# Kernel tuning notes

Hardware: AMD Instinct MI355X
Metric: run time of the kernel (lower is better)

The kernel has to match this reference:

```python
import jax, jax.numpy as jnp
import numpy as np

N_NODES = 100000   # batch of target nodes
K = 10             # sampled neighbors per node (num_sample default)
VOCAB = 200000     # total graph nodes in embedding table
D = 128            # embed_dim


def setup_inputs() -> dict:
    key = jax.random.key(0)
    k1, k2, k3 = jax.random.split(key, 3)
    embed_table = jax.random.normal(k1, (VOCAB, D), dtype=jnp.float32)
    attn_w = jax.random.normal(k2, (D,), dtype=jnp.float32)
    neigh_idx = jax.random.randint(k3, (N_NODES, K), 0, VOCAB, dtype=jnp.int64)
    return {"embed_table": embed_table, "attn_w": attn_w, "neigh_idx": neigh_idx}


def reference(embed_table, attn_w, neigh_idx):
    # Gather neighbor embeddings: [N, K, D] (the irregular-access hot spot)
    feats = embed_table[neigh_idx]
    # attention_fc: Linear(D, 1, bias=False) -> scores [N, K]
    scores = jnp.einsum("nkd,d->nk", feats, attn_w)
    # softmax over the neighbor axis (dim=0 in the per-node torch loop == K here)
    weights = jax.nn.softmax(scores, axis=1)
    # attention-weighted sum of neighbor features -> [N, D]
    out = jnp.einsum("nk,nkd->nd", weights, feats)
    return out
```

## Files before the change

### kernel.cpp

```cpp
#include <hip/hip_runtime.h>
#include <math.h>


#define KNEIGH 10
#define DIM    128
#define QMAX   126.5f

__global__ __launch_bounds__(256) void convert_q8_kernel(
    const float*  __restrict__ table,
    const float*  __restrict__ attn_w,
    unsigned int* __restrict__ q8,
    float2*       __restrict__ aux,
    int vocab)
{
    const int gtid = blockIdx.x * blockDim.x + threadIdx.x;
    const int lane = threadIdx.x & 63;
    const int half = lane >> 5;
    const int sub  = lane & 31;
    const int row  = (gtid >> 6) * 2 + half;
    if (row >= vocab) return;

    const float4 f  = *(const float4*)(table + (size_t)row * DIM + sub * 4);
    const float4 w4 = *(const float4*)(attn_w + sub * 4);

    float p = f.x * w4.x + f.y * w4.y + f.z * w4.z + f.w * w4.w;
    float am = fmaxf(fmaxf(fabsf(f.x), fabsf(f.y)),
                     fmaxf(fabsf(f.z), fabsf(f.w)));
    #pragma unroll
    for (int off = 16; off >= 1; off >>= 1) {
        p  += __shfl_xor(p, off, 64);
        am  = fmaxf(am, __shfl_xor(am, off, 64));
    }

    const float scale = am * (1.0f / QMAX);
    const float inv   = (am > 0.f) ? (QMAX / am) : 0.f;

    const int q0 = (int)rintf(f.x * inv) + 128;
    const int q1 = (int)rintf(f.y * inv) + 128;
    const int q2 = (int)rintf(f.z * inv) + 128;
    const int q3 = (int)rintf(f.w * inv) + 128;
    q8[(size_t)row * 32 + sub] =
        (unsigned)q0 | ((unsigned)q1 << 8) | ((unsigned)q2 << 16) |
        ((unsigned)q3 << 24);

    if (sub == 0) aux[row] = make_float2(p, scale);
}

__global__ __launch_bounds__(256) void attn_gather_q8_kernel(
    const unsigned int* __restrict__ q8,
    const float2*       __restrict__ aux,
    const int*          __restrict__ idx,
    float*              __restrict__ out,
    int n_nodes)
{
    const int gtid = blockIdx.x * blockDim.x + threadIdx.x;
    const int wid  = gtid >> 6;
    const int n0   = wid * 2;
    if (n0 >= n_nodes) return;
    const int  n1   = n0 + 1;
    const bool has1 = (n1 < n_nodes);
    const int  lane = threadIdx.x & 63;
    const int  q    = lane >> 4;
    const int  sub  = lane & 15;

    const int b0 = __builtin_amdgcn_readfirstlane(n0) * KNEIGH;
    const int b1 = has1 ? b0 + KNEIGH : b0;

    const int ia0 = idx[b0+0], ia1 = idx[b0+1], ia2 = idx[b0+2], ia3 = idx[b0+3],
              ia4 = idx[b0+4], ia5 = idx[b0+5], ia6 = idx[b0+6], ia7 = idx[b0+7],
              ia8 = idx[b0+8], ia9 = idx[b0+9];
    const int ib0 = idx[b1+0], ib1 = idx[b1+1], ib2 = idx[b1+2], ib3 = idx[b1+3],
              ib4 = idx[b1+4], ib5 = idx[b1+5], ib6 = idx[b1+6], ib7 = idx[b1+7],
              ib8 = idx[b1+8], ib9 = idx[b1+9];

    const int r0 = (q == 0) ? ia0 : (q == 1) ? ia1 : (q == 2) ? ia2 : ia3;
    const int r1 = (q == 0) ? ia4 : (q == 1) ? ia5 : (q == 2) ? ia6 : ia7;
    const int r2 = (q == 0) ? ia8 : (q == 1) ? ia9 : (q == 2) ? ib0 : ib1;
    const int r3 = (q == 0) ? ib2 : (q == 1) ? ib3 : (q == 2) ? ib4 : ib5;
    const int r4 = (q == 0) ? ib6 : (q == 1) ? ib7 : (q == 2) ? ib8 : ib9;

    const uint2 g0 = *(const uint2*)(q8 + (size_t)r0 * 32 + sub * 2);
    const uint2 g1 = *(const uint2*)(q8 + (size_t)r1 * 32 + sub * 2);
    const uint2 g2 = *(const uint2*)(q8 + (size_t)r2 * 32 + sub * 2);
    const uint2 g3 = *(const uint2*)(q8 + (size_t)r3 * 32 + sub * 2);
    const uint2 g4 = *(const uint2*)(q8 + (size_t)r4 * 32 + sub * 2);

    const float2 aa0 = aux[ia0], aa1 = aux[ia1], aa2 = aux[ia2],
                 aa3 = aux[ia3], aa4 = aux[ia4], aa5 = aux[ia5],
                 aa6 = aux[ia6], aa7 = aux[ia7], aa8 = aux[ia8],
                 aa9 = aux[ia9];
    const float2 ab0 = aux[ib0], ab1 = aux[ib1], ab2 = aux[ib2],
                 ab3 = aux[ib3], ab4 = aux[ib4], ab5 = aux[ib5],
                 ab6 = aux[ib6], ab7 = aux[ib7], ab8 = aux[ib8],
                 ab9 = aux[ib9];

    float sa0 = aa0.x, sa1 = aa1.x, sa2 = aa2.x, sa3 = aa3.x, sa4 = aa4.x,
          sa5 = aa5.x, sa6 = aa6.x, sa7 = aa7.x, sa8 = aa8.x, sa9 = aa9.x;
    float ma = fmaxf(fmaxf(fmaxf(fmaxf(sa0, sa1), fmaxf(sa2, sa3)),
                           fmaxf(fmaxf(sa4, sa5), fmaxf(sa6, sa7))),
                     fmaxf(sa8, sa9));
    sa0 = __expf(sa0 - ma); sa1 = __expf(sa1 - ma); sa2 = __expf(sa2 - ma);
    sa3 = __expf(sa3 - ma); sa4 = __expf(sa4 - ma); sa5 = __expf(sa5 - ma);
    sa6 = __expf(sa6 - ma); sa7 = __expf(sa7 - ma); sa8 = __expf(sa8 - ma);
    sa9 = __expf(sa9 - ma);
    const float inva = 1.0f /
        (sa0 + sa1 + sa2 + sa3 + sa4 + sa5 + sa6 + sa7 + sa8 + sa9);

    float sb0 = ab0.x, sb1 = ab1.x, sb2 = ab2.x, sb3 = ab3.x, sb4 = ab4.x,
          sb5 = ab5.x, sb6 = ab6.x, sb7 = ab7.x, sb8 = ab8.x, sb9 = ab9.x;
    float mb = fmaxf(fmaxf(fmaxf(fmaxf(sb0, sb1), fmaxf(sb2, sb3)),
                           fmaxf(fmaxf(sb4, sb5), fmaxf(sb6, sb7))),
                     fmaxf(sb8, sb9));
    sb0 = __expf(sb0 - mb); sb1 = __expf(sb1 - mb); sb2 = __expf(sb2 - mb);
    sb3 = __expf(sb3 - mb); sb4 = __expf(sb4 - mb); sb5 = __expf(sb5 - mb);
    sb6 = __expf(sb6 - mb); sb7 = __expf(sb7 - mb); sb8 = __expf(sb8 - mb);
    sb9 = __expf(sb9 - mb);
    const float invb = 1.0f /
        (sb0 + sb1 + sb2 + sb3 + sb4 + sb5 + sb6 + sb7 + sb8 + sb9);

    const float ta0 = sa0 * inva * aa0.y, ta1 = sa1 * inva * aa1.y,
                ta2 = sa2 * inva * aa2.y, ta3 = sa3 * inva * aa3.y,
                ta4 = sa4 * inva * aa4.y, ta5 = sa5 * inva * aa5.y,
                ta6 = sa6 * inva * aa6.y, ta7 = sa7 * inva * aa7.y,
                ta8 = sa8 * inva * aa8.y, ta9 = sa9 * inva * aa9.y;
    const float tb0 = sb0 * invb * ab0.y, tb1 = sb1 * invb * ab1.y,
                tb2 = sb2 * invb * ab2.y, tb3 = sb3 * invb * ab3.y,
                tb4 = sb4 * invb * ab4.y, tb5 = sb5 * invb * ab5.y,
                tb6 = sb6 * invb * ab6.y, tb7 = sb7 * invb * ab7.y,
                tb8 = sb8 * invb * ab8.y, tb9 = sb9 * invb * ab9.y;

    const float Ca = -128.f * (ta0 + ta1 + ta2 + ta3 + ta4 +
                               ta5 + ta6 + ta7 + ta8 + ta9);
    const float Cb = -128.f * (tb0 + tb1 + tb2 + tb3 + tb4 +
                               tb5 + tb6 + tb7 + tb8 + tb9);

    const float w0 = (q == 0) ? ta0 : (q == 1) ? ta1 : (q == 2) ? ta2 : ta3;
    const float w1 = (q == 0) ? ta4 : (q == 1) ? ta5 : (q == 2) ? ta6 : ta7;
    const float w2 = (q == 0) ? ta8 : (q == 1) ? ta9 : (q == 2) ? tb0 : tb1;
    const float w3 = (q == 0) ? tb2 : (q == 1) ? tb3 : (q == 2) ? tb4 : tb5;
    const float w4 = (q == 0) ? tb6 : (q == 1) ? tb7 : (q == 2) ? tb8 : tb9;

    float a0=0.f,a1=0.f,a2=0.f,a3=0.f,a4=0.f,a5=0.f,a6=0.f,a7=0.f;
    float b0f=0.f,b1f=0.f,b2f=0.f,b3f=0.f,b4f=0.f,b5f=0.f,b6f=0.f,b7f=0.f;

    #define UNPK(G, W, A0,A1,A2,A3,A4,A5,A6,A7)                                \
        A0 = fmaf((W), (float)((G).x & 0xffu),         A0);                    \
        A1 = fmaf((W), (float)(((G).x >> 8) & 0xffu),  A1);                    \
        A2 = fmaf((W), (float)(((G).x >> 16) & 0xffu), A2);                    \
        A3 = fmaf((W), (float)((G).x >> 24),           A3);                    \
        A4 = fmaf((W), (float)((G).y & 0xffu),         A4);                    \
        A5 = fmaf((W), (float)(((G).y >> 8) & 0xffu),  A5);                    \
        A6 = fmaf((W), (float)(((G).y >> 16) & 0xffu), A6);                    \
        A7 = fmaf((W), (float)((G).y >> 24),           A7);

    UNPK(g0, w0, a0,a1,a2,a3,a4,a5,a6,a7)
    UNPK(g1, w1, a0,a1,a2,a3,a4,a5,a6,a7)
    {
        float c0=0.f,c1=0.f,c2=0.f,c3=0.f,c4=0.f,c5=0.f,c6=0.f,c7=0.f;
        UNPK(g2, w2, c0,c1,c2,c3,c4,c5,c6,c7)
        const bool lo = (q < 2);
        a0 += lo ? c0 : 0.f; a1 += lo ? c1 : 0.f; a2 += lo ? c2 : 0.f;
        a3 += lo ? c3 : 0.f; a4 += lo ? c4 : 0.f; a5 += lo ? c5 : 0.f;
        a6 += lo ? c6 : 0.f; a7 += lo ? c7 : 0.f;
        b0f += lo ? 0.f : c0; b1f += lo ? 0.f : c1; b2f += lo ? 0.f : c2;
        b3f += lo ? 0.f : c3; b4f += lo ? 0.f : c4; b5f += lo ? 0.f : c5;
        b6f += lo ? 0.f : c6; b7f += lo ? 0.f : c7;
    }
    UNPK(g3, w3, b0f,b1f,b2f,b3f,b4f,b5f,b6f,b7f)
    UNPK(g4, w4, b0f,b1f,b2f,b3f,b4f,b5f,b6f,b7f)
    #undef UNPK

    #define RED(X) X += __shfl_xor(X, 16, 64); X += __shfl_xor(X, 32, 64);
    RED(a0) RED(a1) RED(a2) RED(a3) RED(a4) RED(a5) RED(a6) RED(a7)
    RED(b0f) RED(b1f) RED(b2f) RED(b3f) RED(b4f) RED(b5f) RED(b6f) RED(b7f)
    #undef RED

    if (q == 0) {
        float* p = out + (size_t)n0 * DIM + sub * 8;
        *(float4*)(p)     = make_float4(a0 + Ca, a1 + Ca, a2 + Ca, a3 + Ca);
        *(float4*)(p + 4) = make_float4(a4 + Ca, a5 + Ca, a6 + Ca, a7 + Ca);
    } else if (q == 1 && has1) {
        float* p = out + (size_t)n1 * DIM + sub * 8;
        *(float4*)(p)     = make_float4(b0f + Cb, b1f + Cb, b2f + Cb, b3f + Cb);
        *(float4*)(p + 4) = make_float4(b4f + Cb, b5f + Cb, b6f + Cb, b7f + Cb);
    }
}

__global__ __launch_bounds__(256) void attn_agg_fp32_kernel(
    const float* __restrict__ table,
    const float* __restrict__ attn_w,
    const int*   __restrict__ idx,
    float*       __restrict__ out,
    int n_nodes)
{
    const int gtid = blockIdx.x * blockDim.x + threadIdx.x;
    const int node = gtid >> 6;
    const int lane = threadIdx.x & 63;
    if (node >= n_nodes) return;

    const float2 wv = *(const float2*)(attn_w + lane * 2);
    int my_idx = 0;
    if (lane < KNEIGH) my_idx = idx[node * KNEIGH + lane];

    float2 f[KNEIGH];
    float  s[KNEIGH];
    #pragma unroll
    for (int k = 0; k < KNEIGH; ++k) {
        const int id = __shfl(my_idx, k, 64);
        f[k] = *(const float2*)(table + (size_t)id * DIM + lane * 2);
        float p = f[k].x * wv.x + f[k].y * wv.y;
        #pragma unroll
        for (int off = 32; off >= 1; off >>= 1)
            p += __shfl_xor(p, off, 64);
        s[k] = p;
    }
    float m = s[0];
    #pragma unroll
    for (int k = 1; k < KNEIGH; ++k) m = fmaxf(m, s[k]);
    float denom = 0.f;
    #pragma unroll
    for (int k = 0; k < KNEIGH; ++k) { s[k] = __expf(s[k] - m); denom += s[k]; }
    const float inv = 1.0f / denom;
    float2 acc = make_float2(0.f, 0.f);
    #pragma unroll
    for (int k = 0; k < KNEIGH; ++k) {
        const float wk = s[k] * inv;
        acc.x = fmaf(wk, f[k].x, acc.x);
        acc.y = fmaf(wk, f[k].y, acc.y);
    }
    *(float2*)(out + (size_t)node * DIM + lane * 2) = acc;
}

extern "C" void kernel_launch(void* const* d_in, const int* in_sizes, int n_in,
                              void* d_out, int out_size, void* d_ws, size_t ws_size,
                              hipStream_t stream) {
    const float* table  = (const float*)d_in[0];
    const float* attn_w = (const float*)d_in[1];
    const int*   idx    = (const int*)d_in[2];
    float*       out    = (float*)d_out;

    const int vocab   = in_sizes[0] / DIM;
    const int n_nodes = in_sizes[2] / KNEIGH;

    const size_t q8_bytes = (size_t)vocab * DIM;
    const size_t need     = q8_bytes + (size_t)vocab * sizeof(float2);

    if (ws_size >= need) {
        unsigned int* q8  = (unsigned int*)d_ws;
        float2*       aux = (float2*)((char*)d_ws + q8_bytes);

        const int waves1  = (vocab + 1) / 2;
        const int blocks1 = (waves1 + 3) / 4;
        convert_q8_kernel<<<blocks1, 256, 0, stream>>>(
            table, attn_w, q8, aux, vocab);

        const int waves2  = (n_nodes + 1) / 2;
        const int blocks2 = (waves2 + 3) / 4;
        attn_gather_q8_kernel<<<blocks2, 256, 0, stream>>>(
            q8, aux, idx, out, n_nodes);
    } else {
        const int blocks = (n_nodes + 3) / 4;
        attn_agg_fp32_kernel<<<blocks, 256, 0, stream>>>(
            table, attn_w, idx, out, n_nodes);
    }
}
```

Before: 197.2 us.

## Split softmax weight computation into separate per-node kernel before gather

Moves the per-node softmax over the neighbor scores into a new kernel that runs one thread per node and writes normalized, scale-folded weights plus an offset constant to a workspace buffer. The gather kernel then reads 12 precomputed floats per node instead of redundantly computing 20 aux gathers, exps and reductions in every lane of the wave. The gather kernel also gets a launch-bounds occupancy hint. The cost is an extra kernel launch and an extra round trip through workspace memory for the weights.

Measured after the change: 194.7 us. No clear change (-1.3%).

```diff
diff --git a/kernel.cpp b/kernel.cpp
--- a/kernel.cpp
+++ b/kernel.cpp
@@ -2,9 +2,10 @@
 #include <math.h>
 
 
-#define KNEIGH 10
-#define DIM    128
-#define QMAX   126.5f
+#define KNEIGH  10
+#define DIM     128
+#define QMAX    126.5f
+#define WSTRIDE 12
 
 __global__ __launch_bounds__(256) void convert_q8_kernel(
     const float*  __restrict__ table,
@@ -46,16 +47,56 @@
     if (sub == 0) aux[row] = make_float2(p, scale);
 }
 
-__global__ __launch_bounds__(256) void attn_gather_q8_kernel(
+__global__ __launch_bounds__(256) void weights_kernel(
+    const float2* __restrict__ aux,
+    const int*    __restrict__ idx,
+    float*        __restrict__ wt,
+    int n_nodes)
+{
+    const int node = blockIdx.x * blockDim.x + threadIdx.x;
+    if (node >= n_nodes) return;
+
+    const int2* ip = (const int2*)(idx + (size_t)node * KNEIGH);
+    const int2 i01 = ip[0], i23 = ip[1], i45 = ip[2], i67 = ip[3], i89 = ip[4];
+
+    const float2 a0 = aux[i01.x], a1 = aux[i01.y], a2 = aux[i23.x],
+                 a3 = aux[i23.y], a4 = aux[i45.x], a5 = aux[i45.y],
+                 a6 = aux[i67.x], a7 = aux[i67.y], a8 = aux[i89.x],
+                 a9 = aux[i89.y];
+
+    const float m = fmaxf(fmaxf(fmaxf(fmaxf(a0.x, a1.x), fmaxf(a2.x, a3.x)),
+                                fmaxf(fmaxf(a4.x, a5.x), fmaxf(a6.x, a7.x))),
+                          fmaxf(a8.x, a9.x));
+    const float e0 = __expf(a0.x - m), e1 = __expf(a1.x - m),
+                e2 = __expf(a2.x - m), e3 = __expf(a3.x - m),
+                e4 = __expf(a4.x - m), e5 = __expf(a5.x - m),
+                e6 = __expf(a6.x - m), e7 = __expf(a7.x - m),
+                e8 = __expf(a8.x - m), e9 = __expf(a9.x - m);
+    const float inv = 1.0f / (e0 + e1 + e2 + e3 + e4 + e5 + e6 + e7 + e8 + e9);
+
+    const float t0 = e0 * inv * a0.y, t1 = e1 * inv * a1.y,
+                t2 = e2 * inv * a2.y, t3 = e3 * inv * a3.y,
+                t4 = e4 * inv * a4.y, t5 = e5 * inv * a5.y,
+                t6 = e6 * inv * a6.y, t7 = e7 * inv * a7.y,
+                t8 = e8 * inv * a8.y, t9 = e9 * inv * a9.y;
+    const float C = -128.f * (t0 + t1 + t2 + t3 + t4 + t5 + t6 + t7 + t8 + t9);
+
+    float4* wp = (float4*)(wt + (size_t)node * WSTRIDE);
+    wp[0] = make_float4(t0, t1, t2, t3);
+    wp[1] = make_float4(t4, t5, t6, t7);
+    wp[2] = make_float4(t8, t9, C, 0.f);
+}
+
+__global__ __launch_bounds__(256, 8) void attn_gather_q8_kernel(
     const unsigned int* __restrict__ q8,
-    const float2*       __restrict__ aux,
+    const float*        __restrict__ wt,
     const int*          __restrict__ idx,
     float*              __restrict__ out,
     int n_nodes)
 {
     const int gtid = blockIdx.x * blockDim.x + threadIdx.x;
     const int wid  = gtid >> 6;
-    const int n0   = wid * 2;
+    const int n0   = __builtin_amdgcn_readfirstlane(wid * 2);
     if (n0 >= n_nodes) return;
     const int  n1   = n0 + 1;
     const bool has1 = (n1 < n_nodes);
@@ -63,7 +104,7 @@
     const int  q    = lane >> 4;
     const int  sub  = lane & 15;
 
-    const int b0 = __builtin_amdgcn_readfirstlane(n0) * KNEIGH;
+    const int b0 = n0 * KNEIGH;
     const int b1 = has1 ? b0 + KNEIGH : b0;
 
     const int ia0 = idx[b0+0], ia1 = idx[b0+1], ia2 = idx[b0+2], ia3 = idx[b0+3],
@@ -85,54 +126,14 @@
     const uint2 g3 = *(const uint2*)(q8 + (size_t)r3 * 32 + sub * 2);
     const uint2 g4 = *(const uint2*)(q8 + (size_t)r4 * 32 + sub * 2);
 
-    const float2 aa0 = aux[ia0], aa1 = aux[ia1], aa2 = aux[ia2],
-                 aa3 = aux[ia3], aa4 = aux[ia4], aa5 = aux[ia5],
-                 aa6 = aux[ia6], aa7 = aux[ia7], aa8 = aux[ia8],
-                 aa9 = aux[ia9];
-    const float2 ab0 = aux[ib0], ab1 = aux[ib1], ab2 = aux[ib2],
-                 ab3 = aux[ib3], ab4 = aux[ib4], ab5 = aux[ib5],
-                 ab6 = aux[ib6], ab7 = aux[ib7], ab8 = aux[ib8],
-                 ab9 = aux[ib9];
-
-    float sa0 = aa0.x, sa1 = aa1.x, sa2 = aa2.x, sa3 = aa3.x, sa4 = aa4.x,
-          sa5 = aa5.x, sa6 = aa6.x, sa7 = aa7.x, sa8 = aa8.x, sa9 = aa9.x;
-    float ma = fmaxf(fmaxf(fmaxf(fmaxf(sa0, sa1), fmaxf(sa2, sa3)),
-                           fmaxf(fmaxf(sa4, sa5), fmaxf(sa6, sa7))),
-                     fmaxf(sa8, sa9));
-    sa0 = __expf(sa0 - ma); sa1 = __expf(sa1 - ma); sa2 = __expf(sa2 - ma);
-    sa3 = __expf(sa3 - ma); sa4 = __expf(sa4 - ma); sa5 = __expf(sa5 - ma);
-    sa6 = __expf(sa6 - ma); sa7 = __expf(sa7 - ma); sa8 = __expf(sa8 - ma);
-    sa9 = __expf(sa9 - ma);
-    const float inva = 1.0f /
-        (sa0 + sa1 + sa2 + sa3 + sa4 + sa5 + sa6 + sa7 + sa8 + sa9);
-
-    float sb0 = ab0.x, sb1 = ab1.x, sb2 = ab2.x, sb3 = ab3.x, sb4 = ab4.x,
-          sb5 = ab5.x, sb6 = ab6.x, sb7 = ab7.x, sb8 = ab8.x, sb9 = ab9.x;
-    float mb = fmaxf(fmaxf(fmaxf(fmaxf(sb0, sb1), fmaxf(sb2, sb3)),
-                           fmaxf(fmaxf(sb4, sb5), fmaxf(sb6, sb7))),
-                     fmaxf(sb8, sb9));
-    sb0 = __expf(sb0 - mb); sb1 = __expf(sb1 - mb); sb2 = __expf(sb2 - mb);
-    sb3 = __expf(sb3 - mb); sb4 = __expf(sb4 - mb); sb5 = __expf(sb5 - mb);
-    sb6 = __expf(sb6 - mb); sb7 = __expf(sb7 - mb); sb8 = __expf(sb8 - mb);
-    sb9 = __expf(sb9 - mb);
-    const float invb = 1.0f /
-        (sb0 + sb1 + sb2 + sb3 + sb4 + sb5 + sb6 + sb7 + sb8 + sb9);
-
-    const float ta0 = sa0 * inva * aa0.y, ta1 = sa1 * inva * aa1.y,
-                ta2 = sa2 * inva * aa2.y, ta3 = sa3 * inva * aa3.y,
-                ta4 = sa4 * inva * aa4.y, ta5 = sa5 * inva * aa5.y,
-                ta6 = sa6 * inva * aa6.y, ta7 = sa7 * inva * aa7.y,
-                ta8 = sa8 * inva * aa8.y, ta9 = sa9 * inva * aa9.y;
-    const float tb0 = sb0 * invb * ab0.y, tb1 = sb1 * invb * ab1.y,
-                tb2 = sb2 * invb * ab2.y, tb3 = sb3 * invb * ab3.y,
-                tb4 = sb4 * invb * ab4.y, tb5 = sb5 * invb * ab5.y,
-                tb6 = sb6 * invb * ab6.y, tb7 = sb7 * invb * ab7.y,
-                tb8 = sb8 * invb * ab8.y, tb9 = sb9 * invb * ab9.y;
-
-    const float Ca = -128.f * (ta0 + ta1 + ta2 + ta3 + ta4 +
-                               ta5 + ta6 + ta7 + ta8 + ta9);
-    const float Cb = -128.f * (tb0 + tb1 + tb2 + tb3 + tb4 +
-                               tb5 + tb6 + tb7 + tb8 + tb9);
+    const float* wa = wt + (size_t)n0 * WSTRIDE;
+    const float* wb = wt + (size_t)(has1 ? n1 : n0) * WSTRIDE;
+    const float ta0 = wa[0], ta1 = wa[1], ta2 = wa[2], ta3 = wa[3],
+                ta4 = wa[4], ta5 = wa[5], ta6 = wa[6], ta7 = wa[7],
+                ta8 = wa[8], ta9 = wa[9], Ca = wa[10];
+    const float tb0 = wb[0], tb1 = wb[1], tb2 = wb[2], tb3 = wb[3],
+                tb4 = wb[4], tb5 = wb[5], tb6 = wb[6], tb7 = wb[7],
+                tb8 = wb[8], tb9 = wb[9], Cb = wb[10];
 
     const float w0 = (q == 0) ? ta0 : (q == 1) ? ta1 : (q == 2) ? ta2 : ta3;
     const float w1 = (q == 0) ? ta4 : (q == 1) ? ta5 : (q == 2) ? ta6 : ta7;
@@ -242,22 +243,29 @@
     const int vocab   = in_sizes[0] / DIM;
     const int n_nodes = in_sizes[2] / KNEIGH;
 
-    const size_t q8_bytes = (size_t)vocab * DIM;
-    const size_t need     = q8_bytes + (size_t)vocab * sizeof(float2);
+    const size_t q8_bytes  = (size_t)vocab * DIM;
+    const size_t aux_bytes = (size_t)vocab * sizeof(float2);
+    const size_t wt_bytes  = (size_t)n_nodes * WSTRIDE * sizeof(float);
+    const size_t need      = q8_bytes + aux_bytes + wt_bytes;
 
     if (ws_size >= need) {
         unsigned int* q8  = (unsigned int*)d_ws;
         float2*       aux = (float2*)((char*)d_ws + q8_bytes);
+        float*        wt  = (float*)((char*)d_ws + q8_bytes + aux_bytes);
 
         const int waves1  = (vocab + 1) / 2;
         const int blocks1 = (waves1 + 3) / 4;
         convert_q8_kernel<<<blocks1, 256, 0, stream>>>(
             table, attn_w, q8, aux, vocab);
 
+        const int blocksW = (n_nodes + 255) / 256;
+        weights_kernel<<<blocksW, 256, 0, stream>>>(
+            aux, idx, wt, n_nodes);
+
         const int waves2  = (n_nodes + 1) / 2;
         const int blocks2 = (waves2 + 3) / 4;
         attn_gather_q8_kernel<<<blocks2, 256, 0, stream>>>(
-            q8, aux, idx, out, n_nodes);
+            q8, wt, idx, out, n_nodes);
     } else {
         const int blocks = (n_nodes + 3) / 4;
         attn_agg_fp32_kernel<<<blocks, 256, 0, stream>>>(
```
